# Performance work log

Hardware: AMD Instinct MI355X
Metric: run time of the kernel (lower is better)

The kernel has to match this reference:

```python
import jax, jax.numpy as jnp
import numpy as np

EPS = 1e-12  # torch F.normalize eps

def _l2norm(x):
    n = jnp.linalg.norm(x, axis=1, keepdims=True)
    return x / jnp.maximum(n, EPS)

def setup_inputs() -> dict:
    key = jax.random.key(0)
    kq, km = jax.random.split(key)
    queries = jax.random.normal(kq, (4096, 128), dtype=jnp.float32)
    memory = jax.random.normal(km, (100000, 128), dtype=jnp.float32)
    return {"queries": queries, "memory": memory, "k": 3}

def reference(queries, memory, k):
    q = _l2norm(queries)                      # [N, D]
    m = _l2norm(memory)                       # [M, D]
    sims = q @ m.T                            # [N, M]
    values, indices = jax.lax.top_k(sims, k)  # [N, k] each
    distances = 1.0 - values
    return distances, indices
```

## Files before the change

kernel.cpp:

```cpp
#include <hip/hip_runtime.h>
#include <hip/hip_bf16.h>

typedef unsigned short u16;
typedef unsigned int u32;

#define N_Q 4096
#define N_M 100000
#define N_M_PAD 100096
#define DDIM 128
#define QTILE 128
#define MTILE 64
#define NCHUNK 16
#define NQT (N_Q / QTILE)
#define TOTAL_MT (N_M_PAD / MTILE)
#define TPC ((TOTAL_MT + NCHUNK - 1) / NCHUNK)
#define NCAND (NCHUNK * 2 * 3)

typedef short bf16x8 __attribute__((ext_vector_type(8)));
typedef float f32x4 __attribute__((ext_vector_type(4)));

static __device__ __forceinline__ u16 f2bf(float v) {
  union { float f; u32 u; } a; a.f = v;
  u32 r = a.u + 0x7fffu + ((a.u >> 16) & 1u);
  return (u16)(r >> 16);
}

static __device__ __forceinline__ void async_copy16(const u16* gp, u16* lp) {
  __builtin_amdgcn_global_load_lds(
      (const __attribute__((address_space(1))) u32*)gp,
      (__attribute__((address_space(3))) u32*)lp, 16, 0, 0);
}

__global__ __launch_bounds__(256) void knorm(const float* __restrict__ q, const float* __restrict__ m,
                                             u16* __restrict__ qn, u16* __restrict__ mn,
                                             float* __restrict__ qinv, float* __restrict__ minv) {
  const int lane = threadIdx.x & 63;
  const int nw = gridDim.x * 4;
  for (int row = blockIdx.x * 4 + (threadIdx.x >> 6); row < N_Q + N_M_PAD; row += nw) {
    const float* src;
    u16* dst;
    int mr = 0;
    bool is_q = (row < N_Q);
    bool pad = false;
    if (is_q) {
      src = q + (size_t)row * DDIM;
      dst = qn + (size_t)row * DDIM;
    } else {
      mr = row - N_Q;
      pad = (mr >= N_M);
      src = m + (size_t)mr * DDIM;
      dst = mn + (size_t)mr * DDIM;
    }
    float2 x;
    if (pad) { x.x = 0.f; x.y = 0.f; }
    else x = ((const float2*)src)[lane];
    float s = x.x * x.x + x.y * x.y;
    #pragma unroll
    for (int off = 1; off < 64; off <<= 1) s += __shfl_xor(s, off, 64);
    float invn = 1.0f / fmaxf(sqrtf(s), 1e-12f);
    u32 packed = (u32)f2bf(x.x * invn) | ((u32)f2bf(x.y * invn) << 16);
    ((u32*)dst)[lane] = packed;
    if (lane == 0) {
      if (is_q) qinv[row] = invn;
      else minv[mr] = pad ? 0.f : invn;
    }
  }
}

static __device__ __forceinline__ void stage4(const u16* __restrict__ mn, u16* dst,
                                              int t, const u32* goff, u32 loff0) {
  const u16* gbase = mn + (size_t)t * MTILE * DDIM;
  #pragma unroll
  for (int it = 0; it < 4; ++it)
    async_copy16(gbase + goff[it], dst + loff0 + (u32)(it * 64) * 8);
}

static __device__ __forceinline__ void tileWork(
    const u16* As, int tl, int wm, int quad, int l15,
    const bf16x8 (&bq)[4][4], float (&tv0)[4], float (&tv1)[4], float (&tv2)[4]) {
  f32x4 acc[2][4];
  {
    int c = quad ^ l15;
    bf16x8 a0 = *(const bf16x8*)&As[((wm * 32 + l15) * 16 + c) * 8];
    bf16x8 a1 = *(const bf16x8*)&As[((wm * 32 + 16 + l15) * 16 + c) * 8];
    f32x4 z = {0.f, 0.f, 0.f, 0.f};
    #pragma unroll
    for (int ni = 0; ni < 4; ++ni) {
      acc[0][ni] = __builtin_amdgcn_mfma_f32_16x16x32_bf16(a0, bq[ni][0], z, 0, 0, 0);
      acc[1][ni] = __builtin_amdgcn_mfma_f32_16x16x32_bf16(a1, bq[ni][0], z, 0, 0, 0);
    }
  }
  #pragma unroll
  for (int s = 1; s < 4; ++s) {
    int c = (s * 4 + quad) ^ l15;
    bf16x8 a0 = *(const bf16x8*)&As[((wm * 32 + l15) * 16 + c) * 8];
    bf16x8 a1 = *(const bf16x8*)&As[((wm * 32 + 16 + l15) * 16 + c) * 8];
    #pragma unroll
    for (int ni = 0; ni < 4; ++ni) {
      acc[0][ni] = __builtin_amdgcn_mfma_f32_16x16x32_bf16(a0, bq[ni][s], acc[0][ni], 0, 0, 0);
      acc[1][ni] = __builtin_amdgcn_mfma_f32_16x16x32_bf16(a1, bq[ni][s], acc[1][ni], 0, 0, 0);
    }
  }
  const u32 code = ((u32)tl << 2) | (u32)quad;
  #pragma unroll
  for (int ni = 0; ni < 4; ++ni) {
    f32x4 x0 = acc[0][ni], x1 = acc[1][ni];
    float M = fmaxf(fmaxf(fmaxf(x0[0], x0[1]), fmaxf(x0[2], x0[3])),
                    fmaxf(fmaxf(x1[0], x1[1]), fmaxf(x1[2], x1[3])));
    float pk = __uint_as_float((__float_as_uint(M) & 0xFFFFFE00u) | code);
    tv2[ni] = __builtin_amdgcn_fmed3f(tv1[ni], tv2[ni], pk);
    tv1[ni] = __builtin_amdgcn_fmed3f(tv0[ni], tv1[ni], pk);
    tv0[ni] = fmaxf(tv0[ni], pk);
  }
}

__global__ __launch_bounds__(256, 2) void kgemm(const u16* __restrict__ qn,
                                                const u16* __restrict__ mn,
                                                float* __restrict__ pval) {
  __shared__ u16 B0[MTILE * DDIM];
  __shared__ u16 B1[MTILE * DDIM];
  __shared__ u16 B2[MTILE * DDIM];
  __shared__ u16 B3[MTILE * DDIM];

  const int id = blockIdx.x;
  const int xcd = id & 7, sub = id >> 3;
  const int ch = xcd * 2 + (sub >> 5);
  const int qt = sub & 31;
  const int tid = threadIdx.x;
  const int wid = tid >> 6, lane = tid & 63;
  const int quad = lane >> 4, l15 = lane & 15;
  const int wm = wid >> 1, wq = wid & 1;

  const int t0 = ch * TPC;
  const int t1 = (t0 + TPC < TOTAL_MT) ? (t0 + TPC) : TOTAL_MT;
  const int nt = t1 - t0;

  u32 goff[4];
  u32 loff0;
  {
    int u0 = wid * 256 + lane;
    loff0 = (u32)(wid * 256) * 8;
    #pragma unroll
    for (int it = 0; it < 4; ++it) {
      int u = u0 + it * 64;
      int row = u >> 4, su = u & 15;
      int k8 = su ^ (row & 15);
      goff[it] = (u32)(row * DDIM + k8 * 8);
    }
  }

  stage4(mn, B0, t0 + 0, goff, loff0);
  stage4(mn, B1, t0 + 1, goff, loff0);
  stage4(mn, B2, t0 + 2, goff, loff0);

  bf16x8 bq[4][4];
  #pragma unroll
  for (int ni = 0; ni < 4; ++ni) {
    int col = qt * QTILE + wq * 64 + ni * 16 + l15;
    #pragma unroll
    for (int s = 0; s < 4; ++s)
      bq[ni][s] = *(const bf16x8*)&qn[(size_t)col * DDIM + (s * 4 + quad) * 8];
  }

  float tv0[4], tv1[4], tv2[4];
  #pragma unroll
  for (int i = 0; i < 4; ++i) { tv0[i] = tv1[i] = tv2[i] = -1e30f; }

  asm volatile("s_waitcnt vmcnt(0)" ::: "memory");
  asm volatile("s_barrier" ::: "memory");

  int r = 0;
  #define ROUND(BC, BS)                                                        \
    {                                                                          \
      int ts = t0 + r + 3;                                                     \
      ts = (ts < t1) ? ts : (t1 - 1);                                          \
      stage4(mn, BS, ts, goff, loff0);                                         \
      tileWork(BC, r, wm, quad, l15, bq, tv0, tv1, tv2);                       \
      asm volatile("s_waitcnt vmcnt(8)" ::: "memory");                         \
      asm volatile("s_barrier" ::: "memory");                                  \
      ++r;                                                                     \
      if (r >= nt) break;                                                      \
    }
  while (true) {
    ROUND(B0, B3)
    ROUND(B1, B0)
    ROUND(B2, B1)
    ROUND(B3, B2)
  }
  #undef ROUND

  #pragma unroll
  for (int ni = 0; ni < 4; ++ni) {
    float a0 = tv0[ni], a1 = tv1[ni], a2 = tv2[ni];
    #pragma unroll
    for (int off = 16; off <= 32; off <<= 1) {
      float b0 = __shfl_xor(a0, off, 64);
      float b1 = __shfl_xor(a1, off, 64);
      float b2 = __shfl_xor(a2, off, 64);
      float n0 = fmaxf(a0, b0);
      float n1 = __builtin_amdgcn_fmed3f(a0, b0, fmaxf(a1, b1));
      float n2 = fmaxf(fmaxf(fminf(a1, b0), fminf(a0, b1)), fmaxf(a2, b2));
      a0 = n0; a1 = n1; a2 = n2;
    }
    float v = (quad == 0) ? a0 : ((quad == 1) ? a1 : a2);
    if (quad < 3) {
      int qlocal = wq * 64 + ni * 16 + l15;
      size_t base = (((size_t)qt * NCHUNK + ch) * QTILE + qlocal) * 6 + wm * 3 + quad;
      pval[base] = v;
    }
  }
}

__global__ __launch_bounds__(256) void kmerge(const float* __restrict__ pval,
                                              const float* __restrict__ q,
                                              const float* __restrict__ mem,
                                              const float* __restrict__ qinv,
                                              const float* __restrict__ minv,
                                              float* __restrict__ out) {
  __shared__ float sv[4][64];
  const int tid = threadIdx.x;
  const int wq = tid >> 6;
  const int lane = tid & 63;
  const int qg = blockIdx.x * 4 + wq;
  const int qt = qg >> 7, ql = qg & 127;

  const int c0 = lane * 2;
  float cv[2] = {-1e31f, -1e31f};
  if (c0 < NCAND) {
    int chn = c0 / 6, rem = c0 - chn * 6;
    size_t b = (((size_t)qt * NCHUNK + chn) * QTILE + ql) * 6 + rem;
    cv[0] = pval[b];
    cv[1] = pval[b + 1];
  }

  float wv[8]; int wp[8];
  #pragma unroll
  for (int pass = 0; pass < 8; ++pass) {
    float bv = cv[0]; int bp = c0;
    bool g1 = (cv[1] > bv);
    bv = g1 ? cv[1] : bv; bp = g1 ? (c0 + 1) : bp;
    #pragma unroll
    for (int off = 32; off >= 1; off >>= 1) {
      float ov = __shfl_xor(bv, off, 64);
      int op = __shfl_xor(bp, off, 64);
      bool g = (ov > bv) || (ov == bv && op < bp);
      bv = g ? ov : bv; bp = g ? op : bp;
    }
    wv[pass] = bv; wp[pass] = bp;
    if (c0 == bp) cv[0] = -1e31f;
    if (c0 + 1 == bp) cv[1] = -1e31f;
  }

  const float qi = qinv[qg];
  const float* qrow = q + (size_t)qg * DDIM;
  const int e = lane >> 3, f = lane & 7;

  #pragma unroll
  for (int p = 0; p < 8; ++p) {
    int bp = wp[p];
    u32 code = __float_as_uint(wv[p]) & 511u;
    int chn = bp / 6;
    int wm = (bp - chn * 6) / 3;
    int tl = (int)(code >> 2), qd = (int)(code & 3u);
    int row = (chn * TPC + tl) * MTILE + wm * 32 + (e >> 2) * 16 + qd * 4 + (e & 3);
    bool valid = (row < N_M);
    int ra = valid ? row : 0;
    const float* mrow = mem + (size_t)ra * DDIM;
    float s = 0.f;
    #pragma unroll
    for (int i = 0; i < 4; ++i) {
      float4 mv = *(const float4*)&mrow[(f + 8 * i) * 4];
      float4 qv = *(const float4*)&qrow[(f + 8 * i) * 4];
      s += qv.x * mv.x + qv.y * mv.y + qv.z * mv.z + qv.w * mv.w;
    }
    #pragma unroll
    for (int off = 1; off < 8; off <<= 1) s += __shfl_xor(s, off, 64);
    s = valid ? (s * qi * minv[ra]) : -1e30f;
    if (f == 0) sv[wq][p * 8 + e] = s;
  }
  __syncthreads();

  float myv = sv[wq][lane];
  {
    int p = lane >> 3, e2 = lane & 7;
    int bp = wp[p];
    u32 code = __float_as_uint(wv[p]) & 511u;
    int chn = bp / 6;
    int wm = (bp - chn * 6) / 3;
    int tl = (int)(code >> 2), qd = (int)(code & 3u);
    int row = (chn * TPC + tl) * MTILE + wm * 32 + (e2 >> 2) * 16 + qd * 4 + (e2 & 3);
    int myrow = (row < N_M) ? row : (N_M + lane);

    #pragma unroll
    for (int a = 0; a < 3; ++a) {
      float bv = myv; int bi = myrow;
      #pragma unroll
      for (int off = 32; off >= 1; off >>= 1) {
        float ov = __shfl_xor(bv, off, 64);
        int oi = __shfl_xor(bi, off, 64);
        bool g2 = (ov > bv) || (ov == bv && oi < bi);
        bv = g2 ? ov : bv; bi = g2 ? oi : bi;
      }
      if (lane == 0) {
        out[(size_t)qg * 3 + a] = 1.0f - bv;
        out[(size_t)N_Q * 3 + (size_t)qg * 3 + a] = (float)bi;
      }
      if (myrow == bi) myv = -1e31f;
    }
  }
}

extern "C" void kernel_launch(void* const* d_in, const int* in_sizes, int n_in,
                              void* d_out, int out_size, void* d_ws, size_t ws_size,
                              hipStream_t stream) {
  const float* q = (const float*)d_in[0];
  const float* m = (const float*)d_in[1];

  char* ws = (char*)d_ws;
  size_t off = 0;
  u16* qn = (u16*)(ws + off); off += (size_t)N_Q * DDIM * 2;
  u16* mn = (u16*)(ws + off); off += (size_t)N_M_PAD * DDIM * 2;
  float* qinv = (float*)(ws + off); off += (size_t)N_Q * 4;
  float* minv = (float*)(ws + off); off += (size_t)N_M_PAD * 4;
  float* pval = (float*)(ws + off); off += (size_t)N_Q * NCAND * 4;

  knorm<<<1024, 256, 0, stream>>>(q, m, qn, mn, qinv, minv);
  kgemm<<<NQT * NCHUNK, 256, 0, stream>>>(qn, mn, pval);
  kmerge<<<N_Q / 4, 256, 0, stream>>>(pval, q, m, qinv, minv, (float*)d_out);
}
```

Before: 213.1 us.

## Raise GEMM occupancy with triple-buffering, more chunks, and finer candidate codes

The memory tiles are now split into 24 chunks instead of 16, and each GEMM block keeps three LDS buffers instead of four so three blocks can share a CU. Candidate packing now tracks 16-row groups instead of 32-row groups, and the merge kernel rescoring is reorganised to match: 8 winners with 4 rows each, split across two lanes per row. Dropping one stage of prefetch gives the loads less time to hide behind compute. Stealing one more mantissa bit for the packed index slightly changes how values compare. The knorm grid is also doubled.

```diff
diff --git a/kernel.cpp b/kernel.cpp
--- a/kernel.cpp
+++ b/kernel.cpp
@@ -10,7 +10,7 @@
 #define DDIM 128
 #define QTILE 128
 #define MTILE 64
-#define NCHUNK 16
+#define NCHUNK 24
 #define NQT (N_Q / QTILE)
 #define TOTAL_MT (N_M_PAD / MTILE)
 #define TPC ((TOTAL_MT + NCHUNK - 1) / NCHUNK)
@@ -101,30 +101,31 @@
       acc[1][ni] = __builtin_amdgcn_mfma_f32_16x16x32_bf16(a1, bq[ni][s], acc[1][ni], 0, 0, 0);
     }
   }
-  const u32 code = ((u32)tl << 2) | (u32)quad;
+  const u32 cb = ((u32)tl << 3) | ((u32)quad << 1);
   #pragma unroll
   for (int ni = 0; ni < 4; ++ni) {
-    f32x4 x0 = acc[0][ni], x1 = acc[1][ni];
-    float M = fmaxf(fmaxf(fmaxf(x0[0], x0[1]), fmaxf(x0[2], x0[3])),
-                    fmaxf(fmaxf(x1[0], x1[1]), fmaxf(x1[2], x1[3])));
-    float pk = __uint_as_float((__float_as_uint(M) & 0xFFFFFE00u) | code);
-    tv2[ni] = __builtin_amdgcn_fmed3f(tv1[ni], tv2[ni], pk);
-    tv1[ni] = __builtin_amdgcn_fmed3f(tv0[ni], tv1[ni], pk);
-    tv0[ni] = fmaxf(tv0[ni], pk);
-  }
-}
-
-__global__ __launch_bounds__(256, 2) void kgemm(const u16* __restrict__ qn,
+    #pragma unroll
+    for (int mi = 0; mi < 2; ++mi) {
+      f32x4 x = acc[mi][ni];
+      float M = fmaxf(fmaxf(x[0], x[1]), fmaxf(x[2], x[3]));
+      float pk = __uint_as_float((__float_as_uint(M) & 0xFFFFFC00u) | (cb | (u32)mi));
+      tv2[ni] = __builtin_amdgcn_fmed3f(tv1[ni], tv2[ni], pk);
+      tv1[ni] = __builtin_amdgcn_fmed3f(tv0[ni], tv1[ni], pk);
+      tv0[ni] = fmaxf(tv0[ni], pk);
+    }
+  }
+}
+
+__global__ __launch_bounds__(256, 3) void kgemm(const u16* __restrict__ qn,
                                                 const u16* __restrict__ mn,
                                                 float* __restrict__ pval) {
   __shared__ u16 B0[MTILE * DDIM];
   __shared__ u16 B1[MTILE * DDIM];
   __shared__ u16 B2[MTILE * DDIM];
-  __shared__ u16 B3[MTILE * DDIM];
 
   const int id = blockIdx.x;
   const int xcd = id & 7, sub = id >> 3;
-  const int ch = xcd * 2 + (sub >> 5);
+  const int ch = xcd * 3 + (sub >> 5);
   const int qt = sub & 31;
   const int tid = threadIdx.x;
   const int wid = tid >> 6, lane = tid & 63;
@@ -149,43 +150,41 @@
     }
   }
 
+  bf16x8 bq[4][4];
+  #pragma unroll
+  for (int ni = 0; ni < 4; ++ni) {
+    int col = qt * QTILE + wq * 64 + ni * 16 + l15;
+    #pragma unroll
+    for (int s = 0; s < 4; ++s)
+      bq[ni][s] = *(const bf16x8*)&qn[(size_t)col * DDIM + (s * 4 + quad) * 8];
+  }
+
   stage4(mn, B0, t0 + 0, goff, loff0);
   stage4(mn, B1, t0 + 1, goff, loff0);
-  stage4(mn, B2, t0 + 2, goff, loff0);
-
-  bf16x8 bq[4][4];
-  #pragma unroll
-  for (int ni = 0; ni < 4; ++ni) {
-    int col = qt * QTILE + wq * 64 + ni * 16 + l15;
-    #pragma unroll
-    for (int s = 0; s < 4; ++s)
-      bq[ni][s] = *(const bf16x8*)&qn[(size_t)col * DDIM + (s * 4 + quad) * 8];
-  }
 
   float tv0[4], tv1[4], tv2[4];
   #pragma unroll
   for (int i = 0; i < 4; ++i) { tv0[i] = tv1[i] = tv2[i] = -1e30f; }
 
-  asm volatile("s_waitcnt vmcnt(0)" ::: "memory");
+  asm volatile("s_waitcnt vmcnt(4)" ::: "memory");
   asm volatile("s_barrier" ::: "memory");
 
   int r = 0;
   #define ROUND(BC, BS)                                                        \
     {                                                                          \
-      int ts = t0 + r + 3;                                                     \
+      int ts = t0 + r + 2;                                                     \
       ts = (ts < t1) ? ts : (t1 - 1);                                          \
       stage4(mn, BS, ts, goff, loff0);                                         \
       tileWork(BC, r, wm, quad, l15, bq, tv0, tv1, tv2);                       \
-      asm volatile("s_waitcnt vmcnt(8)" ::: "memory");                         \
+      asm volatile("s_waitcnt vmcnt(4)" ::: "memory");                         \
       asm volatile("s_barrier" ::: "memory");                                  \
       ++r;                                                                     \
       if (r >= nt) break;                                                      \
     }
   while (true) {
-    ROUND(B0, B3)
+    ROUND(B0, B2)
     ROUND(B1, B0)
     ROUND(B2, B1)
-    ROUND(B3, B2)
   }
   #undef ROUND
 
@@ -217,28 +216,32 @@
                                               const float* __restrict__ qinv,
                                               const float* __restrict__ minv,
                                               float* __restrict__ out) {
-  __shared__ float sv[4][64];
+  __shared__ float sv[4][32];
   const int tid = threadIdx.x;
-  const int wq = tid >> 6;
+  const int wqd = tid >> 6;
   const int lane = tid & 63;
-  const int qg = blockIdx.x * 4 + wq;
+  const int qg = blockIdx.x * 4 + wqd;
   const int qt = qg >> 7, ql = qg & 127;
 
-  const int c0 = lane * 2;
-  float cv[2] = {-1e31f, -1e31f};
+  const int c0 = lane * 3;
+  float cv[3] = {-1e31f, -1e31f, -1e31f};
   if (c0 < NCAND) {
     int chn = c0 / 6, rem = c0 - chn * 6;
     size_t b = (((size_t)qt * NCHUNK + chn) * QTILE + ql) * 6 + rem;
     cv[0] = pval[b];
     cv[1] = pval[b + 1];
+    cv[2] = pval[b + 2];
   }
 
   float wv[8]; int wp[8];
   #pragma unroll
   for (int pass = 0; pass < 8; ++pass) {
     float bv = cv[0]; int bp = c0;
-    bool g1 = (cv[1] > bv);
-    bv = g1 ? cv[1] : bv; bp = g1 ? (c0 + 1) : bp;
+    #pragma unroll
+    for (int j = 1; j < 3; ++j) {
+      bool g = (cv[j] > bv);
+      bv = g ? cv[j] : bv; bp = g ? (c0 + j) : bp;
+    }
     #pragma unroll
     for (int off = 32; off >= 1; off >>= 1) {
       float ov = __shfl_xor(bv, off, 64);
@@ -247,66 +250,78 @@
       bv = g ? ov : bv; bp = g ? op : bp;
     }
     wv[pass] = bv; wp[pass] = bp;
-    if (c0 == bp) cv[0] = -1e31f;
-    if (c0 + 1 == bp) cv[1] = -1e31f;
+    #pragma unroll
+    for (int j = 0; j < 3; ++j)
+      if (c0 + j == bp) cv[j] = -1e31f;
   }
 
   const float qi = qinv[qg];
   const float* qrow = q + (size_t)qg * DDIM;
-  const int e = lane >> 3, f = lane & 7;
-
-  #pragma unroll
-  for (int p = 0; p < 8; ++p) {
-    int bp = wp[p];
-    u32 code = __float_as_uint(wv[p]) & 511u;
-    int chn = bp / 6;
-    int wm = (bp - chn * 6) / 3;
-    int tl = (int)(code >> 2), qd = (int)(code & 3u);
-    int row = (chn * TPC + tl) * MTILE + wm * 32 + (e >> 2) * 16 + qd * 4 + (e & 3);
+
+  const int p = lane >> 3, e = (lane >> 1) & 3, h = lane & 1;
+  float bvv = wv[0]; int bpp = wp[0];
+  #pragma unroll
+  for (int k = 1; k < 8; ++k) {
+    bvv = (p == k) ? wv[k] : bvv;
+    bpp = (p == k) ? wp[k] : bpp;
+  }
+  {
+    u32 code = __float_as_uint(bvv) & 1023u;
+    int chn = bpp / 6;
+    int wm = (bpp - chn * 6) / 3;
+    int tl = (int)(code >> 3), qd = (int)((code >> 1) & 3u), mi = (int)(code & 1u);
+    int row = (chn * TPC + tl) * MTILE + wm * 32 + mi * 16 + qd * 4 + e;
     bool valid = (row < N_M);
     int ra = valid ? row : 0;
     const float* mrow = mem + (size_t)ra * DDIM;
     float s = 0.f;
     #pragma unroll
-    for (int i = 0; i < 4; ++i) {
-      float4 mv = *(const float4*)&mrow[(f + 8 * i) * 4];
-      float4 qv = *(const float4*)&qrow[(f + 8 * i) * 4];
+    for (int i = 0; i < 16; ++i) {
+      float4 mv = *(const float4*)&mrow[h * 64 + i * 4];
+      float4 qv = *(const float4*)&qrow[h * 64 + i * 4];
       s += qv.x * mv.x + qv.y * mv.y + qv.z * mv.z + qv.w * mv.w;
     }
-    #pragma unroll
-    for (int off = 1; off < 8; off <<= 1) s += __shfl_xor(s, off, 64);
+    s += __shfl_xor(s, 1, 64);
     s = valid ? (s * qi * minv[ra]) : -1e30f;
-    if (f == 0) sv[wq][p * 8 + e] = s;
+    if (h == 0) sv[wqd][p * 4 + e] = s;
   }
   __syncthreads();
 
-  float myv = sv[wq][lane];
+  float myv = (lane < 32) ? sv[wqd][lane] : -1e31f;
+  int myrow;
   {
-    int p = lane >> 3, e2 = lane & 7;
-    int bp = wp[p];
-    u32 code = __float_as_uint(wv[p]) & 511u;
-    int chn = bp / 6;
-    int wm = (bp - chn * 6) / 3;
-    int tl = (int)(code >> 2), qd = (int)(code & 3u);
-    int row = (chn * TPC + tl) * MTILE + wm * 32 + (e2 >> 2) * 16 + qd * 4 + (e2 & 3);
-    int myrow = (row < N_M) ? row : (N_M + lane);
-
-    #pragma unroll
-    for (int a = 0; a < 3; ++a) {
-      float bv = myv; int bi = myrow;
-      #pragma unroll
-      for (int off = 32; off >= 1; off >>= 1) {
-        float ov = __shfl_xor(bv, off, 64);
-        int oi = __shfl_xor(bi, off, 64);
-        bool g2 = (ov > bv) || (ov == bv && oi < bi);
-        bv = g2 ? ov : bv; bi = g2 ? oi : bi;
-      }
-      if (lane == 0) {
-        out[(size_t)qg * 3 + a] = 1.0f - bv;
-        out[(size_t)N_Q * 3 + (size_t)qg * 3 + a] = (float)bi;
-      }
-      if (myrow == bi) myv = -1e31f;
-    }
+    int p2 = lane >> 2, e2 = lane & 3;
+    float bv2 = wv[0]; int bp2 = wp[0];
+    #pragma unroll
+    for (int k = 1; k < 8; ++k) {
+      bool sel = (p2 == k);
+      bv2 = sel ? wv[k] : bv2;
+      bp2 = sel ? wp[k] : bp2;
+    }
+    u32 code = __float_as_uint(bv2) & 1023u;
+    int chn = bp2 / 6;
+    int wm = (bp2 - chn * 6) / 3;
+    int tl = (int)(code >> 3), qd = (int)((code >> 1) & 3u), mi = (int)(code & 1u);
+    int row = (chn * TPC + tl) * MTILE + wm * 32 + mi * 16 + qd * 4 + e2;
+    myrow = (lane < 32 && row < N_M) ? row : (N_M + lane);
+    if (lane >= 32 || row >= N_M) myv = -1e31f;
+  }
+
+  #pragma unroll
+  for (int a = 0; a < 3; ++a) {
+    float bv = myv; int bi = myrow;
+    #pragma unroll
+    for (int off = 32; off >= 1; off >>= 1) {
+      float ov = __shfl_xor(bv, off, 64);
+      int oi = __shfl_xor(bi, off, 64);
+      bool g2 = (ov > bv) || (ov == bv && oi < bi);
+      bv = g2 ? ov : bv; bi = g2 ? oi : bi;
+    }
+    if (lane == 0) {
+      out[(size_t)qg * 3 + a] = 1.0f - bv;
+      out[(size_t)N_Q * 3 + (size_t)qg * 3 + a] = (float)bi;
+    }
+    if (myrow == bi) myv = -1e31f;
   }
 }
 
@@ -324,7 +339,7 @@
   float* minv = (float*)(ws + off); off += (size_t)N_M_PAD * 4;
   float* pval = (float*)(ws + off); off += (size_t)N_Q * NCAND * 4;
 
-  knorm<<<1024, 256, 0, stream>>>(q, m, qn, mn, qinv, minv);
+  knorm<<<2048, 256, 0, stream>>>(q, m, qn, mn, qinv, minv);
   kgemm<<<NQT * NCHUNK, 256, 0, stream>>>(qn, mn, pval);
   kmerge<<<N_Q / 4, 256, 0, stream>>>(pval, q, m, qinv, minv, (float*)d_out);
 }
```

Result: slower. 219.3 us (+2.9%).
